# Kernel optimization log

Hardware: AMD Instinct MI355X
Metric: run time of the kernel (lower is better)

## Reference

```python
import jax, jax.numpy as jnp
import numpy as np

D_MODEL = 1024
NUM_HEADS = 16


def setup_inputs() -> dict:
    key = jax.random.key(0)
    ks = jax.random.split(key, 9)
    B, S, D = 4, 1024, D_MODEL
    scale = 1.0 / np.sqrt(D)
    inp = {
        "query": jax.random.normal(ks[0], (B, S, D), dtype=jnp.float32),
        "key": jax.random.normal(ks[1], (B, S, D), dtype=jnp.float32),
        "value": jax.random.normal(ks[2], (B, S, D), dtype=jnp.float32),
        # causal mask: 1 = attend, 0 = blocked (masked_fill where mask==0)
        "mask": jnp.tril(jnp.ones((S, S), dtype=jnp.int32))[None, None, :, :],
        "Wq": jax.random.normal(ks[3], (D, D), dtype=jnp.float32) * scale,
        "Wk": jax.random.normal(ks[4], (D, D), dtype=jnp.float32) * scale,
        "Wv": jax.random.normal(ks[5], (D, D), dtype=jnp.float32) * scale,
        "Wo": jax.random.normal(ks[6], (D, D), dtype=jnp.float32) * scale,
        "bo": jnp.zeros((D,), dtype=jnp.float32),
    }
    return inp


def reference(query, key, value, mask, Wq, Wk, Wv, Wo, bo):
    B, S, D = query.shape
    H = NUM_HEADS
    dk = D // H
    # torch Linear: y = x @ W.T  (bias=False for q/k/v)
    def proj(x, W):
        return (x @ W.T).reshape(B, S, H, dk).transpose(0, 2, 1, 3)  # [B,H,S,dk]

    Q = proj(query, Wq)
    K = proj(key, Wk)
    V = proj(value, Wv)

    scores = jnp.einsum("bhqd,bhkd->bhqk", Q, K) / jnp.sqrt(
        jnp.asarray(dk, dtype=jnp.float32)
    )
    scores = jnp.where(mask == 0, jnp.asarray(-1e9, scores.dtype), scores)
    attn = jax.nn.softmax(scores, axis=-1)
    out = jnp.einsum("bhqk,bhkd->bhqd", attn, V)  # [B,H,S,dk]
    out = out.transpose(0, 2, 1, 3).reshape(B, S, D)
    return out @ Wo.T + bo
```

## Files before the change

### kernel.cpp

```cpp
#include <hip/hip_runtime.h>

typedef __bf16 bf16x8 __attribute__((ext_vector_type(8)));
typedef short  s16x8  __attribute__((ext_vector_type(8)));
typedef float  f32x4  __attribute__((ext_vector_type(4)));
typedef float  f32x16 __attribute__((ext_vector_type(16)));
typedef unsigned int   u32x4 __attribute__((ext_vector_type(4)));
typedef unsigned short u16x4 __attribute__((ext_vector_type(4)));

#define NH   16
#define HD   64
#define SEQ  1024
#define DM   1024
#define NB   4
#define MTOT 4096

#define SCALE_L2E 0.1803368801111204f

__device__ __forceinline__ unsigned short f2bf(float f) {
    unsigned u = __builtin_bit_cast(unsigned, f);
    u += 0x7FFFu + ((u >> 16) & 1u);
    return (unsigned short)(u >> 16);
}

__device__ __forceinline__ s16x8 cvt8(f32x4 a, f32x4 b) {
    s16x8 r;
    r[0] = (short)f2bf(a[0]); r[1] = (short)f2bf(a[1]);
    r[2] = (short)f2bf(a[2]); r[3] = (short)f2bf(a[3]);
    r[4] = (short)f2bf(b[0]); r[5] = (short)f2bf(b[1]);
    r[6] = (short)f2bf(b[2]); r[7] = (short)f2bf(b[3]);
    return r;
}

__device__ __forceinline__ unsigned short bfbits(float x) {
    __bf16 h = (__bf16)x;
    return __builtin_bit_cast(unsigned short, h);
}
__device__ __forceinline__ unsigned pk2(float a, float b) {
    return (unsigned)bfbits(a) | ((unsigned)bfbits(b) << 16);
}

__device__ __forceinline__ void gl16(const void* g, void* l) {
    __builtin_amdgcn_global_load_lds(
        (const __attribute__((address_space(1))) unsigned int*)g,
        (__attribute__((address_space(3))) unsigned int*)l, 16, 0, 0);
}

__global__ __launch_bounds__(256)
void cvt_kernel(const float* __restrict__ q, const float* __restrict__ k,
                const float* __restrict__ v, const float* __restrict__ wq,
                const float* __restrict__ wk, const float* __restrict__ wv,
                const float* __restrict__ wo,
                unsigned short* __restrict__ dq, unsigned short* __restrict__ dk,
                unsigned short* __restrict__ dv, unsigned short* __restrict__ dwq,
                unsigned short* __restrict__ dwk, unsigned short* __restrict__ dwv,
                unsigned short* __restrict__ dwo)
{
    const int id = blockIdx.x;
    const float* s; unsigned short* d; int off; float scl = 1.0f;
    if (id < 6144) {
        const int t = id >> 11; off = id & 2047;
        s = (t == 0) ? q : (t == 1) ? k : v;
        d = (t == 0) ? dq : (t == 1) ? dk : dv;
    } else {
        const int w = (id - 6144) >> 9; off = (id - 6144) & 511;
        s = (w == 0) ? wq : (w == 1) ? wk : (w == 2) ? wv : wo;
        d = (w == 0) ? dwq : (w == 1) ? dwk : (w == 2) ? dwv : dwo;
        if (w == 0) scl = SCALE_L2E;
    }
    const int idx = off * 2048 + threadIdx.x * 8;
    const f32x4* sp = (const f32x4*)(s + idx);
    *(s16x8*)(d + idx) = cvt8(sp[0] * scl, sp[1] * scl);
}

__device__ __forceinline__ void stage128x64(const unsigned short* __restrict__ src,
                                            int row0, int k0, char* lds, int tid)
{
    const int wv  = tid >> 6;
    const int row = tid >> 3;
    const int scx = ((tid & 7) * 16) ^ ((row & 7) << 4);
    #pragma unroll
    for (int i = 0; i < 4; ++i) {
        const char* g = (const char*)(src + (size_t)(row0 + i * 32 + row) * DM + k0) + scx;
        gl16(g, lds + i * 4096 + wv * 1024);
    }
}

__device__ __forceinline__ void stage_half(const unsigned short* __restrict__ src,
                                           int grow0, int k0, char* ldsdst, int tid)
{
    const int wv  = tid >> 6;
    const int row = tid >> 3;
    const int scx = ((tid & 7) * 16) ^ ((row & 7) << 4);
    gl16((const char*)(src + (size_t)(grow0 + row) * DM + k0) + scx,
         ldsdst + wv * 1024);
    gl16((const char*)(src + (size_t)(grow0 + 64 + row) * DM + k0) + scx,
         ldsdst + 8192 + wv * 1024);
}

__device__ __forceinline__ bf16x8 ldfrag(const char* base, int row, int cb) {
    return __builtin_bit_cast(bf16x8,
        *(const s16x8*)(base + row * 128 + (cb ^ ((row & 7) << 4))));
}

__global__ __launch_bounds__(512, 2)
void proj_kernel(const unsigned short* __restrict__ Xq,
                 const unsigned short* __restrict__ Xk,
                 const unsigned short* __restrict__ Xv,
                 const unsigned short* __restrict__ Wq,
                 const unsigned short* __restrict__ Wk,
                 const unsigned short* __restrict__ Wv,
                 unsigned short* __restrict__ Qo, unsigned short* __restrict__ Ko,
                 unsigned short* __restrict__ VTo)
{
    __shared__ char smem[147456];

    const int bid = blockIdx.x;
    const int swz = (bid & 7) * 24 + (bid >> 3);
    const int which = swz >> 6;
    const int rem   = swz & 63;
    const int m0 = (rem >> 2) * 256, n0 = (rem & 3) * 256;

    const unsigned short* X = (which == 0) ? Xq : (which == 1) ? Xk : Xv;
    const unsigned short* W = (which == 0) ? Wq : (which == 1) ? Wk : Wv;

    const int tid = threadIdx.x, lane = tid & 63, wv = tid >> 6;
    const int wrB = (wv >> 2) * 128;
    const int wcB = (wv & 3) * 64;
    const int fr = lane & 15, hi = lane >> 4, r4 = hi * 4;

    f32x4 acc[8][4];
    #pragma unroll
    for (int i = 0; i < 8; ++i)
        #pragma unroll
        for (int j = 0; j < 4; ++j) acc[i][j] = (f32x4){0.f, 0.f, 0.f, 0.f};

    stage_half(X, m0,       0, smem +     0, tid);
    stage_half(X, m0 + 128, 0, smem + 16384, tid);
    stage_half(W, n0,       0, smem + 32768, tid);
    stage_half(W, n0 + 128, 0, smem + 49152, tid);

    for (int t = 0; t < 16; ++t) {
        const char* Abuf = smem + (t & 1) * 65536;
        const char* Bbuf = Abuf + 32768;
        char* nb = smem + ((t & 1) ^ 1) * 65536;
        const int kn = (t + 1) * 64;

        bf16x8 af[2][4], bf01[2][2], bf23[2][2];

        if (t < 15) {
            stage_half(X, m0, kn, nb, tid);
            asm volatile("s_waitcnt vmcnt(2)" ::: "memory");
        } else {
            asm volatile("s_waitcnt vmcnt(0)" ::: "memory");
        }
        __builtin_amdgcn_s_barrier();
        __builtin_amdgcn_sched_barrier(0);
        #pragma unroll
        for (int ks = 0; ks < 2; ++ks) {
            const int cb = ks * 64 + hi * 16;
            #pragma unroll
            for (int mt = 0; mt < 4; ++mt) af[ks][mt] = ldfrag(Abuf, wrB + mt * 16 + fr, cb);
            #pragma unroll
            for (int nt = 0; nt < 2; ++nt) bf01[ks][nt] = ldfrag(Bbuf, wcB + nt * 16 + fr, cb);
        }
        __builtin_amdgcn_s_setprio(1);
        #pragma unroll
        for (int ks = 0; ks < 2; ++ks)
            #pragma unroll
            for (int mt = 0; mt < 4; ++mt)
                #pragma unroll
                for (int nt = 0; nt < 2; ++nt)
                    acc[mt][nt] = __builtin_amdgcn_mfma_f32_16x16x32_bf16(
                        af[ks][mt], bf01[ks][nt], acc[mt][nt], 0, 0, 0);
        __builtin_amdgcn_s_setprio(0);

        __builtin_amdgcn_s_barrier();
        __builtin_amdgcn_sched_barrier(0);
        #pragma unroll
        for (int ks = 0; ks < 2; ++ks) {
            const int cb = ks * 64 + hi * 16;
            #pragma unroll
            for (int nt = 0; nt < 2; ++nt) bf23[ks][nt] = ldfrag(Bbuf, wcB + 32 + nt * 16 + fr, cb);
        }
        if (t < 15) stage_half(X, m0 + 128, kn, nb + 16384, tid);
        __builtin_amdgcn_s_setprio(1);
        #pragma unroll
        for (int ks = 0; ks < 2; ++ks)
            #pragma unroll
            for (int mt = 0; mt < 4; ++mt)
                #pragma unroll
                for (int nt = 0; nt < 2; ++nt)
                    acc[mt][nt + 2] = __builtin_amdgcn_mfma_f32_16x16x32_bf16(
                        af[ks][mt], bf23[ks][nt], acc[mt][nt + 2], 0, 0, 0);
        __builtin_amdgcn_s_setprio(0);

        __builtin_amdgcn_s_barrier();
        __builtin_amdgcn_sched_barrier(0);
        #pragma unroll
        for (int ks = 0; ks < 2; ++ks) {
            const int cb = ks * 64 + hi * 16;
            #pragma unroll
            for (int mt = 0; mt < 4; ++mt) af[ks][mt] = ldfrag(Abuf, wrB + 64 + mt * 16 + fr, cb);
        }
        if (t < 15) stage_half(W, n0, kn, nb + 32768, tid);
        __builtin_amdgcn_s_setprio(1);
        #pragma unroll
        for (int ks = 0; ks < 2; ++ks)
            #pragma unroll
            for (int mt = 0; mt < 4; ++mt)
                #pragma unroll
                for (int nt = 0; nt < 2; ++nt)
                    acc[mt + 4][nt] = __builtin_amdgcn_mfma_f32_16x16x32_bf16(
                        af[ks][mt], bf01[ks][nt], acc[mt + 4][nt], 0, 0, 0);
        __builtin_amdgcn_s_setprio(0);

        __builtin_amdgcn_s_barrier();
        __builtin_amdgcn_sched_barrier(0);
        if (t < 15) stage_half(W, n0 + 128, kn, nb + 49152, tid);
        __builtin_amdgcn_s_setprio(1);
        #pragma unroll
        for (int ks = 0; ks < 2; ++ks)
            #pragma unroll
            for (int mt = 0; mt < 4; ++mt)
                #pragma unroll
                for (int nt = 0; nt < 2; ++nt)
                    acc[mt + 4][nt + 2] = __builtin_amdgcn_mfma_f32_16x16x32_bf16(
                        af[ks][mt], bf23[ks][nt], acc[mt + 4][nt + 2], 0, 0, 0);
        __builtin_amdgcn_s_setprio(0);
    }

    __syncthreads();

    unsigned short* sE = (unsigned short*)(smem + wv * 18432);
    #pragma unroll
    for (int mt = 0; mt < 8; ++mt)
        #pragma unroll
        for (int nt = 0; nt < 4; ++nt)
            #pragma unroll
            for (int r = 0; r < 4; ++r) {
                const int row = mt * 16 + r4 + r;
                const int col = nt * 16 + fr;
                sE[row * 72 + (col ^ (((row >> 3) & 7) << 3))] = f2bf(acc[mt][nt][r]);
            }
    asm volatile("s_waitcnt lgkmcnt(0)" ::: "memory");

    const int hB    = (n0 + wcB) >> 6;
    const int sbase = m0 + wrB;
    const int bb    = sbase >> 10;
    const int srow0 = sbase & 1023;

    if (which < 2) {
        unsigned short* QK = ((which == 0) ? Qo : Ko)
            + (((size_t)(bb * NH + hB)) * SEQ + srow0) * HD;
        #pragma unroll
        for (int it = 0; it < 16; ++it) {
            const int idx = it * 64 + lane;
            const int row = idx >> 3, c = idx & 7;
            s16x8 v = *(const s16x8*)&sE[row * 72 + ((c ^ ((row >> 3) & 7)) * 8)];
            *(s16x8*)(QK + (size_t)row * HD + c * 8) = v;
        }
    } else {
        unsigned short* VD = VTo + (((size_t)(bb * NH + hB)) * HD) * SEQ + srow0;
        #pragma unroll
        for (int it = 0; it < 16; ++it) {
            const int idx = it * 64 + lane;
            const int d = idx >> 4, sc = idx & 15;
            s16x8 v;
            #pragma unroll
            for (int j = 0; j < 8; ++j) {
                const int row = sc * 8 + j;
                v[j] = (short)sE[row * 72 + (d ^ (((row >> 3) & 7) << 3))];
            }
            *(s16x8*)(VD + (size_t)d * SEQ + sc * 8) = v;
        }
    }
}

#define GEMM_K_LOOP(SRC_A, SRC_B)                                              \
    stage128x64(SRC_A, m0, 0, sA[0], tid);                                     \
    stage128x64(SRC_B, n0, 0, sB[0], tid);                                     \
    for (int kt = 0; kt < 16; ++kt) {                                          \
        const int cur = kt & 1;                                                \
        if (kt < 15) {                                                         \
            stage128x64(SRC_A, m0, (kt + 1) * 64, sA[cur ^ 1], tid);           \
            stage128x64(SRC_B, n0, (kt + 1) * 64, sB[cur ^ 1], tid);           \
            asm volatile("s_waitcnt vmcnt(8)" ::: "memory");                   \
        } else {                                                               \
            asm volatile("s_waitcnt vmcnt(0)" ::: "memory");                   \
        }                                                                      \
        __builtin_amdgcn_s_barrier();                                          \
        __builtin_amdgcn_sched_barrier(0);                                     \
        _Pragma("unroll")                                                      \
        for (int ks = 0; ks < 2; ++ks) {                                       \
            const int cb = ks * 64 + hi * 16;                                  \
            bf16x8 af[4], bfm[4];                                              \
            _Pragma("unroll")                                                  \
            for (int mt = 0; mt < 4; ++mt)                                     \
                af[mt] = ldfrag(sA[cur], wr + mt * 16 + fr, cb);               \
            _Pragma("unroll")                                                  \
            for (int nt = 0; nt < 4; ++nt)                                     \
                bfm[nt] = ldfrag(sB[cur], wc + nt * 16 + fr, cb);              \
            _Pragma("unroll")                                                  \
            for (int mt = 0; mt < 4; ++mt)                                     \
                _Pragma("unroll")                                              \
                for (int nt = 0; nt < 4; ++nt)                                 \
                    acc[mt][nt] = __builtin_amdgcn_mfma_f32_16x16x32_bf16(     \
                        af[mt], bfm[nt], acc[mt][nt], 0, 0, 0);                \
        }                                                                      \
        asm volatile("s_waitcnt lgkmcnt(0)" ::: "memory");                     \
        __builtin_amdgcn_sched_barrier(0);                                     \
        __builtin_amdgcn_s_barrier();                                          \
    }

__global__ __launch_bounds__(256)
void outproj_kernel(const unsigned short* __restrict__ A,
                    const unsigned short* __restrict__ Wo,
                    const float* __restrict__ bo,
                    float* __restrict__ Cout)
{
    const int bid = blockIdx.x;
    const int swz = (bid & 7) * 32 + (bid >> 3);
    const int m0 = (swz >> 3) * 128, n0 = (swz & 7) * 128;

    __shared__ char sA[2][16384];
    __shared__ char sB[2][16384];

    const int tid = threadIdx.x, lane = tid & 63, wv = tid >> 6;
    const int wr = (wv >> 1) * 64, wc = (wv & 1) * 64;
    const int fr = lane & 15, hi = lane >> 4, r4 = hi * 4;

    f32x4 acc[4][4];
    #pragma unroll
    for (int i = 0; i < 4; ++i)
        #pragma unroll
        for (int j = 0; j < 4; ++j) acc[i][j] = (f32x4){0.f, 0.f, 0.f, 0.f};

    GEMM_K_LOOP(A, Wo)

    #pragma unroll
    for (int mt = 0; mt < 4; ++mt)
        #pragma unroll
        for (int nt = 0; nt < 4; ++nt)
            #pragma unroll
            for (int r = 0; r < 4; ++r) {
                int gm = m0 + wr + mt * 16 + r4 + r;
                int gn = n0 + wc + nt * 16 + fr;
                Cout[(size_t)gm * DM + gn] = acc[mt][nt][r] + bo[gn];
            }
}

__global__ __launch_bounds__(256)
void attn_kernel(const unsigned short* __restrict__ Q,
                 const unsigned short* __restrict__ K,
                 const unsigned short* __restrict__ VT,
                 unsigned short* __restrict__ O)
{
    __shared__ unsigned short smem[16384];

    const int bid   = blockIdx.x;
    const int swz   = (bid & 7) * 64 + (bid >> 3);
    const int bh    = swz >> 3;
    const int chunk = 7 - (swz & 7);
    const int q0    = chunk * 128;
    const int tid   = threadIdx.x, lane = tid & 63, wv = tid >> 6;
    const int q0w   = q0 + wv * 32;
    const int ql    = lane & 31;
    const int hi    = lane >> 5;
    const int qg    = q0w + ql;
    const int ndiag = q0w >> 6;
    const int tmax  = 2 * chunk + 2;

    const int srow = tid >> 3;
    const int scx  = ((tid & 7) * 16) ^ ((srow & 7) << 4);

    const unsigned short* Qp = Q + (size_t)bh * SEQ * HD;
    const char* Kc = (const char*)(K  + (size_t)bh * SEQ * HD);
    const char* Vc = (const char*)(VT + (size_t)bh * HD * SEQ);

    bf16x8 qf[4];
    #pragma unroll
    for (int s = 0; s < 4; ++s)
        qf[s] = __builtin_bit_cast(bf16x8,
            *(const s16x8*)(Qp + (size_t)qg * HD + s * 16 + hi * 8));

    f32x16 o0, o1;
    #pragma unroll
    for (int i = 0; i < 16; ++i) { o0[i] = 0.f; o1[i] = 0.f; }
    float mrow = -3.0e38f, lrow = 0.f;

    #pragma unroll
    for (int i = 0; i < 2; ++i) {
        gl16(Kc + (size_t)(srow + i * 32) * 128 + scx,
             (char*)smem + i * 4096 + wv * 1024);
        gl16(Vc + (size_t)(srow + i * 32) * 2048 + scx,
             (char*)smem + 16384 + i * 4096 + wv * 1024);
    }

    for (int t = 0; t < tmax; ++t) {
        const int b = t & 1;
        if (t + 1 < tmax) {
            #pragma unroll
            for (int i = 0; i < 2; ++i) {
                gl16(Kc + (size_t)(t + 1) * 8192 + (size_t)(srow + i * 32) * 128 + scx,
                     (char*)smem + (b ^ 1) * 8192 + i * 4096 + wv * 1024);
                gl16(Vc + (size_t)(srow + i * 32) * 2048 + (size_t)(t + 1) * 128 + scx,
                     (char*)smem + 16384 + (b ^ 1) * 8192 + i * 4096 + wv * 1024);
            }
            asm volatile("s_waitcnt vmcnt(4)" ::: "memory");
        } else {
            asm volatile("s_waitcnt vmcnt(0)" ::: "memory");
        }
        __builtin_amdgcn_s_barrier();
        __builtin_amdgcn_sched_barrier(0);

        if (t <= ndiag) {
            const char* Kb = (const char*)smem + b * 8192;
            const char* Vb = (const char*)smem + 16384 + b * 8192;

            f32x16 s0, s1;
            #pragma unroll
            for (int i = 0; i < 16; ++i) { s0[i] = 0.f; s1[i] = 0.f; }
            #pragma unroll
            for (int s = 0; s < 4; ++s) {
                const int cb = s * 32 + hi * 16;
                const int r0 = ql, r1 = 32 + ql;
                bf16x8 k0 = __builtin_bit_cast(bf16x8,
                    *(const s16x8*)(Kb + r0 * 128 + (cb ^ ((r0 & 7) << 4))));
                bf16x8 k1 = __builtin_bit_cast(bf16x8,
                    *(const s16x8*)(Kb + r1 * 128 + (cb ^ ((r1 & 7) << 4))));
                s0 = __builtin_amdgcn_mfma_f32_32x32x16_bf16(k0, qf[s], s0, 0, 0, 0);
                s1 = __builtin_amdgcn_mfma_f32_32x32x16_bf16(k1, qf[s], s1, 0, 0, 0);
            }

            if (t == ndiag) {
                #pragma unroll
                for (int r = 0; r < 16; ++r) {
                    const int kl = t * 64 + (r & 3) + 8 * (r >> 2) + 4 * hi;
                    s0[r] = (kl      <= qg) ? s0[r] : -3.0e38f;
                    s1[r] = (kl + 32 <= qg) ? s1[r] : -3.0e38f;
                }
            }

            float mt = s0[0];
            #pragma unroll
            for (int r = 1; r < 16; ++r) mt = fmaxf(mt, s0[r]);
            #pragma unroll
            for (int r = 0; r < 16; ++r) mt = fmaxf(mt, s1[r]);
            mt = fmaxf(mt, __shfl_xor(mt, 32, 64));
            const float mnew = fmaxf(mrow, mt);
            const float pc = __builtin_amdgcn_exp2f(mrow - mnew);
            mrow = mnew;

            float ts = 0.f;
            #pragma unroll
            for (int r = 0; r < 16; ++r) { s0[r] = __builtin_amdgcn_exp2f(s0[r] - mnew); ts += s0[r]; }
            #pragma unroll
            for (int r = 0; r < 16; ++r) { s1[r] = __builtin_amdgcn_exp2f(s1[r] - mnew); ts += s1[r]; }
            ts += __shfl_xor(ts, 32, 64);
            lrow = lrow * pc + ts;
            #pragma unroll
            for (int i = 0; i < 16; ++i) { o0[i] *= pc; o1[i] *= pc; }

            #pragma unroll
            for (int s = 0; s < 4; ++s) {
                const f32x16 ps = (s < 2) ? s0 : s1;
                const int bse = (s & 1) * 8;
                unsigned w0 = pk2(ps[bse + 0], ps[bse + 1]);
                unsigned w1 = pk2(ps[bse + 2], ps[bse + 3]);
                unsigned w2 = pk2(ps[bse + 4], ps[bse + 5]);
                unsigned w3 = pk2(ps[bse + 6], ps[bse + 7]);
                unsigned x0 = (unsigned)__shfl_xor((int)(hi ? w0 : w2), 32, 64);
                unsigned x1 = (unsigned)__shfl_xor((int)(hi ? w1 : w3), 32, 64);
                u32x4 fw;
                fw[0] = hi ? x0 : w0;
                fw[1] = hi ? x1 : w1;
                fw[2] = hi ? w2 : x0;
                fw[3] = hi ? w3 : x1;
                const bf16x8 pfrag = __builtin_bit_cast(bf16x8, fw);
                const int cb = s * 32 + hi * 16;
                const int r0 = ql, r1 = 32 + ql;
                bf16x8 v0 = __builtin_bit_cast(bf16x8,
                    *(const s16x8*)(Vb + r0 * 128 + (cb ^ ((r0 & 7) << 4))));
                bf16x8 v1 = __builtin_bit_cast(bf16x8,
                    *(const s16x8*)(Vb + r1 * 128 + (cb ^ ((r1 & 7) << 4))));
                o0 = __builtin_amdgcn_mfma_f32_32x32x16_bf16(v0, pfrag, o0, 0, 0, 0);
                o1 = __builtin_amdgcn_mfma_f32_32x32x16_bf16(v1, pfrag, o1, 0, 0, 0);
            }
        }
        asm volatile("s_waitcnt lgkmcnt(0)" ::: "memory");
        __builtin_amdgcn_sched_barrier(0);
        __builtin_amdgcn_s_barrier();
    }

    const float inv = 1.0f / lrow;
    const int wvb = wv * 2304;
    #pragma unroll
    for (int dt = 0; dt < 2; ++dt) {
        const f32x16 ov = dt ? o1 : o0;
        #pragma unroll
        for (int j = 0; j < 4; ++j) {
            u16x4 w;
            #pragma unroll
            for (int i = 0; i < 4; ++i) w[i] = bfbits(ov[4 * j + i] * inv);
            const int d = dt * 32 + 8 * j + 4 * hi;
            *(u16x4*)&smem[wvb + ql * 72 + d] = w;
        }
    }
    const int bb = bh >> 4, h = bh & 15;
    #pragma unroll
    for (int it = 0; it < 4; ++it) {
        const int idx = it * 64 + lane;
        const int qq = idx >> 3, c = idx & 7;
        s16x8 v = *(const s16x8*)&smem[wvb + qq * 72 + c * 8];
        *(s16x8*)(O + ((size_t)(bb * SEQ + q0w + qq) * DM + h * 64) + c * 8) = v;
    }
}

extern "C" void kernel_launch(void* const* d_in, const int* in_sizes, int n_in,
                              void* d_out, int out_size, void* d_ws, size_t ws_size,
                              hipStream_t stream)
{
    const float* query = (const float*)d_in[0];
    const float* key   = (const float*)d_in[1];
    const float* value = (const float*)d_in[2];
    const float* Wq = (const float*)d_in[4];
    const float* Wk = (const float*)d_in[5];
    const float* Wv = (const float*)d_in[6];
    const float* Wo = (const float*)d_in[7];
    const float* bo = (const float*)d_in[8];
    float* out = (float*)d_out;

    const size_t XE = (size_t)MTOT * DM;
    const size_t WE = (size_t)DM * DM;
    unsigned short* ws16 = (unsigned short*)d_ws;
    unsigned short* Xq16 = ws16;
    unsigned short* Xk16 = Xq16 + XE;
    unsigned short* Xv16 = Xk16 + XE;
    unsigned short* Wq16 = Xv16 + XE;
    unsigned short* Wk16 = Wq16 + WE;
    unsigned short* Wv16 = Wk16 + WE;
    unsigned short* Wo16 = Wv16 + WE;
    unsigned short* Qw   = Wo16 + WE;
    unsigned short* Kw   = Qw + XE;
    unsigned short* VTw  = Kw + XE;
    unsigned short* AO   = VTw + XE;

    cvt_kernel<<<dim3(8192), dim3(256), 0, stream>>>(
        query, key, value, Wq, Wk, Wv, Wo,
        Xq16, Xk16, Xv16, Wq16, Wk16, Wv16, Wo16);

    proj_kernel<<<dim3(192), dim3(512), 0, stream>>>(
        Xq16, Xk16, Xv16, Wq16, Wk16, Wv16, Qw, Kw, VTw);

    attn_kernel<<<dim3(512), dim3(256), 0, stream>>>(Qw, Kw, VTw, AO);

    outproj_kernel<<<dim3(256), dim3(256), 0, stream>>>(AO, Wo16, bo, out);
}
```

Baseline: 106.8 us.

## Split KV tiles across wave pairs in attention with lazy softmax rescaling

Restructures the attention kernel so that each pair of waves shares one 32-row query group. Each wave takes alternating 64-key tiles, stages K into its own LDS slot and reads V straight from global into registers, so block-wide barriers drop out of the loop. The two partial results are merged through LDS with log-sum-exp correction, the grid doubles to 1024 blocks of 64 query rows, and the running max is rescaled only when it grows by more than 8. The risks are extra global traffic for V, wave imbalance on causal diagonals, and a merge epilogue where half the waves sit idle.

```diff
diff --git a/kernel.cpp b/kernel.cpp
--- a/kernel.cpp
+++ b/kernel.cpp
@@ -34,6 +34,10 @@
 __device__ __forceinline__ unsigned short bfbits(float x) {
     __bf16 h = (__bf16)x;
     return __builtin_bit_cast(unsigned short, h);
+}
+__device__ __forceinline__ float bf2f(unsigned short b) {
+    unsigned u = (unsigned)b << 16;
+    return __builtin_bit_cast(float, u);
 }
 __device__ __forceinline__ unsigned pk2(float a, float b) {
     return (unsigned)bfbits(a) | ((unsigned)bfbits(b) << 16);
@@ -349,29 +353,35 @@
             }
 }
 
+__device__ __forceinline__ void stageK64(const char* Kc, int t, char* myK, int lane) {
+    const int krow8 = lane >> 3;
+    const int kcol  = ((lane & 7) * 16) ^ (krow8 << 4);
+    const char* kb = Kc + (size_t)t * 8192;
+    #pragma unroll
+    for (int i = 0; i < 8; ++i)
+        gl16(kb + (i * 8 + krow8) * 128 + kcol, myK + i * 1024);
+}
+
 __global__ __launch_bounds__(256)
 void attn_kernel(const unsigned short* __restrict__ Q,
                  const unsigned short* __restrict__ K,
                  const unsigned short* __restrict__ VT,
                  unsigned short* __restrict__ O)
 {
-    __shared__ unsigned short smem[16384];
-
-    const int bid   = blockIdx.x;
-    const int swz   = (bid & 7) * 64 + (bid >> 3);
-    const int bh    = swz >> 3;
-    const int chunk = 7 - (swz & 7);
-    const int q0    = chunk * 128;
-    const int tid   = threadIdx.x, lane = tid & 63, wv = tid >> 6;
-    const int q0w   = q0 + wv * 32;
-    const int ql    = lane & 31;
-    const int hi    = lane >> 5;
-    const int qg    = q0w + ql;
+    __shared__ char smem[4][8192];
+
+    const int bid = blockIdx.x;
+    const int xcd = bid & 7, idx = bid >> 3;
+    const int bh  = xcd * 8 + (idx & 7);
+    const int rb  = 15 - (idx >> 3);
+    const int tid = threadIdx.x, lane = tid & 63, wv = tid >> 6;
+    const int g = wv >> 1, p = wv & 1;
+    const int q0w = rb * 64 + g * 32;
+    const int ql = lane & 31, hi = lane >> 5;
+    const int qg = q0w + ql;
     const int ndiag = q0w >> 6;
-    const int tmax  = 2 * chunk + 2;
-
-    const int srow = tid >> 3;
-    const int scx  = ((tid & 7) * 16) ^ ((srow & 7) << 4);
+
+    char* myK = smem[wv];
 
     const unsigned short* Qp = Q + (size_t)bh * SEQ * HD;
     const char* Kc = (const char*)(K  + (size_t)bh * SEQ * HD);
@@ -388,131 +398,139 @@
     for (int i = 0; i < 16; ++i) { o0[i] = 0.f; o1[i] = 0.f; }
     float mrow = -3.0e38f, lrow = 0.f;
 
-    #pragma unroll
-    for (int i = 0; i < 2; ++i) {
-        gl16(Kc + (size_t)(srow + i * 32) * 128 + scx,
-             (char*)smem + i * 4096 + wv * 1024);
-        gl16(Vc + (size_t)(srow + i * 32) * 2048 + scx,
-             (char*)smem + 16384 + i * 4096 + wv * 1024);
-    }
-
-    for (int t = 0; t < tmax; ++t) {
-        const int b = t & 1;
-        if (t + 1 < tmax) {
-            #pragma unroll
-            for (int i = 0; i < 2; ++i) {
-                gl16(Kc + (size_t)(t + 1) * 8192 + (size_t)(srow + i * 32) * 128 + scx,
-                     (char*)smem + (b ^ 1) * 8192 + i * 4096 + wv * 1024);
-                gl16(Vc + (size_t)(srow + i * 32) * 2048 + (size_t)(t + 1) * 128 + scx,
-                     (char*)smem + 16384 + (b ^ 1) * 8192 + i * 4096 + wv * 1024);
+    if (p <= ndiag) stageK64(Kc, p, myK, lane);
+
+    for (int t = p; t <= ndiag; t += 2) {
+        asm volatile("s_waitcnt vmcnt(0)" ::: "memory");
+        __builtin_amdgcn_sched_barrier(0);
+
+        f32x16 s0, s1;
+        #pragma unroll
+        for (int i = 0; i < 16; ++i) { s0[i] = 0.f; s1[i] = 0.f; }
+        #pragma unroll
+        for (int s = 0; s < 4; ++s) {
+            const int cb = s * 32 + hi * 16;
+            bf16x8 k0 = ldfrag(myK, ql, cb);
+            bf16x8 k1 = ldfrag(myK, 32 + ql, cb);
+            s0 = __builtin_amdgcn_mfma_f32_32x32x16_bf16(k0, qf[s], s0, 0, 0, 0);
+            s1 = __builtin_amdgcn_mfma_f32_32x32x16_bf16(k1, qf[s], s1, 0, 0, 0);
+        }
+        asm volatile("s_waitcnt lgkmcnt(0)" ::: "memory");
+        __builtin_amdgcn_sched_barrier(0);
+
+        const char* vb = Vc + (size_t)t * 128;
+        s16x8 vr[8];
+        #pragma unroll
+        for (int s = 0; s < 4; ++s) {
+            const int cbB = s * 32 + hi * 16;
+            vr[2 * s]     = *(const s16x8*)(vb + (size_t)ql * 2048 + cbB);
+            vr[2 * s + 1] = *(const s16x8*)(vb + (size_t)(32 + ql) * 2048 + cbB);
+        }
+        if (t + 2 <= ndiag) stageK64(Kc, t + 2, myK, lane);
+
+        if (t == ndiag) {
+            #pragma unroll
+            for (int r = 0; r < 16; ++r) {
+                const int kl = t * 64 + (r & 3) + 8 * (r >> 2) + 4 * hi;
+                s0[r] = (kl      <= qg) ? s0[r] : -3.0e38f;
+                s1[r] = (kl + 32 <= qg) ? s1[r] : -3.0e38f;
             }
-            asm volatile("s_waitcnt vmcnt(4)" ::: "memory");
-        } else {
-            asm volatile("s_waitcnt vmcnt(0)" ::: "memory");
-        }
-        __builtin_amdgcn_s_barrier();
-        __builtin_amdgcn_sched_barrier(0);
-
-        if (t <= ndiag) {
-            const char* Kb = (const char*)smem + b * 8192;
-            const char* Vb = (const char*)smem + 16384 + b * 8192;
-
-            f32x16 s0, s1;
-            #pragma unroll
-            for (int i = 0; i < 16; ++i) { s0[i] = 0.f; s1[i] = 0.f; }
-            #pragma unroll
-            for (int s = 0; s < 4; ++s) {
-                const int cb = s * 32 + hi * 16;
-                const int r0 = ql, r1 = 32 + ql;
-                bf16x8 k0 = __builtin_bit_cast(bf16x8,
-                    *(const s16x8*)(Kb + r0 * 128 + (cb ^ ((r0 & 7) << 4))));
-                bf16x8 k1 = __builtin_bit_cast(bf16x8,
-                    *(const s16x8*)(Kb + r1 * 128 + (cb ^ ((r1 & 7) << 4))));
-                s0 = __builtin_amdgcn_mfma_f32_32x32x16_bf16(k0, qf[s], s0, 0, 0, 0);
-                s1 = __builtin_amdgcn_mfma_f32_32x32x16_bf16(k1, qf[s], s1, 0, 0, 0);
-            }
-
-            if (t == ndiag) {
-                #pragma unroll
-                for (int r = 0; r < 16; ++r) {
-                    const int kl = t * 64 + (r & 3) + 8 * (r >> 2) + 4 * hi;
-                    s0[r] = (kl      <= qg) ? s0[r] : -3.0e38f;
-                    s1[r] = (kl + 32 <= qg) ? s1[r] : -3.0e38f;
-                }
-            }
-
-            float mt = s0[0];
-            #pragma unroll
-            for (int r = 1; r < 16; ++r) mt = fmaxf(mt, s0[r]);
-            #pragma unroll
-            for (int r = 0; r < 16; ++r) mt = fmaxf(mt, s1[r]);
-            mt = fmaxf(mt, __shfl_xor(mt, 32, 64));
+        }
+
+        float mt = s0[0];
+        #pragma unroll
+        for (int r = 1; r < 16; ++r) mt = fmaxf(mt, s0[r]);
+        #pragma unroll
+        for (int r = 0; r < 16; ++r) mt = fmaxf(mt, s1[r]);
+        mt = fmaxf(mt, __shfl_xor(mt, 32, 64));
+
+        if (!__all(mt - mrow <= 8.0f)) {
             const float mnew = fmaxf(mrow, mt);
             const float pc = __builtin_amdgcn_exp2f(mrow - mnew);
             mrow = mnew;
-
-            float ts = 0.f;
-            #pragma unroll
-            for (int r = 0; r < 16; ++r) { s0[r] = __builtin_amdgcn_exp2f(s0[r] - mnew); ts += s0[r]; }
-            #pragma unroll
-            for (int r = 0; r < 16; ++r) { s1[r] = __builtin_amdgcn_exp2f(s1[r] - mnew); ts += s1[r]; }
-            ts += __shfl_xor(ts, 32, 64);
-            lrow = lrow * pc + ts;
+            lrow *= pc;
             #pragma unroll
             for (int i = 0; i < 16; ++i) { o0[i] *= pc; o1[i] *= pc; }
-
-            #pragma unroll
-            for (int s = 0; s < 4; ++s) {
-                const f32x16 ps = (s < 2) ? s0 : s1;
-                const int bse = (s & 1) * 8;
-                unsigned w0 = pk2(ps[bse + 0], ps[bse + 1]);
-                unsigned w1 = pk2(ps[bse + 2], ps[bse + 3]);
-                unsigned w2 = pk2(ps[bse + 4], ps[bse + 5]);
-                unsigned w3 = pk2(ps[bse + 6], ps[bse + 7]);
-                unsigned x0 = (unsigned)__shfl_xor((int)(hi ? w0 : w2), 32, 64);
-                unsigned x1 = (unsigned)__shfl_xor((int)(hi ? w1 : w3), 32, 64);
-                u32x4 fw;
-                fw[0] = hi ? x0 : w0;
-                fw[1] = hi ? x1 : w1;
-                fw[2] = hi ? w2 : x0;
-                fw[3] = hi ? w3 : x1;
-                const bf16x8 pfrag = __builtin_bit_cast(bf16x8, fw);
-                const int cb = s * 32 + hi * 16;
-                const int r0 = ql, r1 = 32 + ql;
-                bf16x8 v0 = __builtin_bit_cast(bf16x8,
-                    *(const s16x8*)(Vb + r0 * 128 + (cb ^ ((r0 & 7) << 4))));
-                bf16x8 v1 = __builtin_bit_cast(bf16x8,
-                    *(const s16x8*)(Vb + r1 * 128 + (cb ^ ((r1 & 7) << 4))));
-                o0 = __builtin_amdgcn_mfma_f32_32x32x16_bf16(v0, pfrag, o0, 0, 0, 0);
-                o1 = __builtin_amdgcn_mfma_f32_32x32x16_bf16(v1, pfrag, o1, 0, 0, 0);
+        }
+
+        float ts = 0.f;
+        #pragma unroll
+        for (int r = 0; r < 16; ++r) { s0[r] = __builtin_amdgcn_exp2f(s0[r] - mrow); ts += s0[r]; }
+        #pragma unroll
+        for (int r = 0; r < 16; ++r) { s1[r] = __builtin_amdgcn_exp2f(s1[r] - mrow); ts += s1[r]; }
+        ts += __shfl_xor(ts, 32, 64);
+        lrow += ts;
+
+        #pragma unroll
+        for (int s = 0; s < 4; ++s) {
+            const f32x16 ps = (s < 2) ? s0 : s1;
+            const int bse = (s & 1) * 8;
+            unsigned w0 = pk2(ps[bse + 0], ps[bse + 1]);
+            unsigned w1 = pk2(ps[bse + 2], ps[bse + 3]);
+            unsigned w2 = pk2(ps[bse + 4], ps[bse + 5]);
+            unsigned w3 = pk2(ps[bse + 6], ps[bse + 7]);
+            unsigned x0 = (unsigned)__shfl_xor((int)(hi ? w0 : w2), 32, 64);
+            unsigned x1 = (unsigned)__shfl_xor((int)(hi ? w1 : w3), 32, 64);
+            u32x4 fw;
+            fw[0] = hi ? x0 : w0;
+            fw[1] = hi ? x1 : w1;
+            fw[2] = hi ? w2 : x0;
+            fw[3] = hi ? w3 : x1;
+            const bf16x8 pfrag = __builtin_bit_cast(bf16x8, fw);
+            o0 = __builtin_amdgcn_mfma_f32_32x32x16_bf16(
+                __builtin_bit_cast(bf16x8, vr[2 * s]), pfrag, o0, 0, 0, 0);
+            o1 = __builtin_amdgcn_mfma_f32_32x32x16_bf16(
+                __builtin_bit_cast(bf16x8, vr[2 * s + 1]), pfrag, o1, 0, 0, 0);
+        }
+    }
+
+    if (p == 1) {
+        unsigned* rec = (unsigned*)smem[wv] + lane * 21;
+        #pragma unroll
+        for (int i = 0; i < 8; ++i) rec[i]     = pk2(o0[2 * i], o0[2 * i + 1]);
+        #pragma unroll
+        for (int i = 0; i < 8; ++i) rec[8 + i] = pk2(o1[2 * i], o1[2 * i + 1]);
+        rec[16] = __builtin_bit_cast(unsigned, mrow);
+        rec[17] = __builtin_bit_cast(unsigned, lrow);
+        asm volatile("s_waitcnt lgkmcnt(0)" ::: "memory");
+    }
+    __syncthreads();
+    if (p == 0) {
+        const unsigned* rec = (const unsigned*)smem[wv + 1] + lane * 21;
+        const float m1 = __builtin_bit_cast(float, rec[16]);
+        const float l1 = __builtin_bit_cast(float, rec[17]);
+        const float ms = fmaxf(mrow, m1);
+        const float c0 = __builtin_amdgcn_exp2f(mrow - ms);
+        const float c1 = __builtin_amdgcn_exp2f(m1 - ms);
+        const float inv = 1.0f / (lrow * c0 + l1 * c1);
+        const float a0 = c0 * inv, a1 = c1 * inv;
+
+        unsigned short* sE = (unsigned short*)smem[wv];
+        #pragma unroll
+        for (int dt = 0; dt < 2; ++dt) {
+            const f32x16 ov = dt ? o1 : o0;
+            #pragma unroll
+            for (int j = 0; j < 4; ++j) {
+                u16x4 w;
+                #pragma unroll
+                for (int i = 0; i < 4; ++i) {
+                    const int ii = 4 * j + i;
+                    const unsigned uw = rec[dt * 8 + (ii >> 1)];
+                    const float pv = bf2f((unsigned short)((ii & 1) ? (uw >> 16) : (uw & 0xffff)));
+                    w[i] = bfbits(ov[ii] * a0 + pv * a1);
+                }
+                *(u16x4*)&sE[ql * 72 + dt * 32 + 8 * j + 4 * hi] = w;
             }
         }
         asm volatile("s_waitcnt lgkmcnt(0)" ::: "memory");
-        __builtin_amdgcn_sched_barrier(0);
-        __builtin_amdgcn_s_barrier();
-    }
-
-    const float inv = 1.0f / lrow;
-    const int wvb = wv * 2304;
-    #pragma unroll
-    for (int dt = 0; dt < 2; ++dt) {
-        const f32x16 ov = dt ? o1 : o0;
-        #pragma unroll
-        for (int j = 0; j < 4; ++j) {
-            u16x4 w;
-            #pragma unroll
-            for (int i = 0; i < 4; ++i) w[i] = bfbits(ov[4 * j + i] * inv);
-            const int d = dt * 32 + 8 * j + 4 * hi;
-            *(u16x4*)&smem[wvb + ql * 72 + d] = w;
-        }
-    }
-    const int bb = bh >> 4, h = bh & 15;
-    #pragma unroll
-    for (int it = 0; it < 4; ++it) {
-        const int idx = it * 64 + lane;
-        const int qq = idx >> 3, c = idx & 7;
-        s16x8 v = *(const s16x8*)&smem[wvb + qq * 72 + c * 8];
-        *(s16x8*)(O + ((size_t)(bb * SEQ + q0w + qq) * DM + h * 64) + c * 8) = v;
+        const int bb = bh >> 4, h = bh & 15;
+        #pragma unroll
+        for (int it = 0; it < 4; ++it) {
+            const int ix = it * 64 + lane;
+            const int qq = ix >> 3, c = ix & 7;
+            s16x8 v = *(const s16x8*)&sE[qq * 72 + c * 8];
+            *(s16x8*)(O + ((size_t)(bb * SEQ + q0w + qq) * DM + h * 64) + c * 8) = v;
+        }
     }
 }
 
@@ -552,7 +570,7 @@
     proj_kernel<<<dim3(192), dim3(512), 0, stream>>>(
         Xq16, Xk16, Xv16, Wq16, Wk16, Wv16, Qw, Kw, VTw);
 
-    attn_kernel<<<dim3(512), dim3(256), 0, stream>>>(Qw, Kw, VTw, AO);
+    attn_kernel<<<dim3(1024), dim3(256), 0, stream>>>(Qw, Kw, VTw, AO);
 
     outproj_kernel<<<dim3(256), dim3(256), 0, stream>>>(AO, Wo16, bo, out);
 }
```

After: 100.6 us. 1.06x faster.
